# Kernel optimization log

Hardware: AMD Instinct MI355X
Metric: run time of the kernel (lower is better)

Reference implementation:

```python
import jax, jax.numpy as jnp
import numpy as np

B, C_IN, C_OUT, N = 8, 256, 256, 2048
SCALE = 10.0
EPSILON = 1e-3
LEAKY_SLOPE = 0.01
NORM_EPS = 1e-12


def setup_inputs() -> dict:
    key = jax.random.key(0)
    k1, k2, k3, k4 = jax.random.split(key, 4)
    query = jax.random.normal(k1, (B, C_IN, N), dtype=jnp.float32)
    key_t = jax.random.normal(k2, (B, C_IN, N), dtype=jnp.float32)
    # Shared key/query conv (self_attention=True), 1x1 Conv1d weights (no bias)
    fan1 = 1.0 / np.sqrt(C_IN)
    fan2 = 1.0 / np.sqrt(2 * C_IN)
    W1 = jax.random.uniform(k3, (2 * C_IN, C_IN), jnp.float32, -fan1, fan1)
    W2 = jax.random.uniform(k4, (C_OUT, 2 * C_IN), jnp.float32, -fan2, fan2)
    return {"query": query, "key": key_t, "W1": W1, "W2": W2}


def _nonlinearity(x, W1, W2):
    # 1x1 Conv1d == channel-mixing matmul; x: [B, C, N]
    h = jnp.einsum("oc,bcn->bon", W1, x)
    h = jnp.where(h >= 0, h, LEAKY_SLOPE * h)
    return jnp.einsum("oc,bcn->bon", W2, h)


def _l2norm(x):
    # F.normalize(x, dim=1): divide by max(||x||_2, eps)
    n = jnp.sqrt(jnp.sum(x * x, axis=1, keepdims=True))
    return x / jnp.maximum(n, NORM_EPS)


def reference(query, key, W1, W2):
    q_out = _l2norm(_nonlinearity(query, W1, W2))  # [B, C_out, Nq]
    k_out = _l2norm(_nonlinearity(key, W1, W2))    # [B, C_out, Nk]
    scores = jnp.einsum("bcq,bck->bqk", q_out, k_out) * SCALE  # [B, Nq, Nk]
    weights = jax.nn.softmax(scores, axis=-1)
    weights = jnp.where(weights > EPSILON, weights, 0.0)  # nn.Threshold(eps, 0)
    return (weights, key)
```

## Files before the change

### kernel.cpp

```cpp
#include <hip/hip_runtime.h>
#include <hip/hip_bf16.h>
#include <math.h>

#define B_      8
#define CIN     256
#define CMID    512
#define COUT    256
#define N_      2048
#define SCALE_  10.0f
#define EPS_THR 1e-3f
#define NORM_EPS_ 1e-12f

typedef __attribute__((ext_vector_type(8))) short short8;
typedef __attribute__((ext_vector_type(4))) float f32x4;

__device__ __forceinline__ ushort f2bf(float x) {
    union { float f; uint u; } v; v.f = x;
    uint r = v.u + 0x7FFF + ((v.u >> 16) & 1);
    return (ushort)(r >> 16);
}
__device__ __forceinline__ float bf2f(ushort h) {
    union { uint u; float f; } v; v.u = ((uint)h) << 16;
    return v.f;
}
__device__ __forceinline__ void gload_lds16(const void* g, void* l) {
    __builtin_amdgcn_global_load_lds((const __attribute__((address_space(1))) void*)g,
                                     (__attribute__((address_space(3))) void*)l, 16, 0, 0);
}

__global__ __launch_bounds__(256) void prep_w(const float* __restrict__ W1,
                                              const float* __restrict__ W2,
                                              ushort* __restrict__ W1b,
                                              ushort* __restrict__ W2b) {
    int idx = blockIdx.x * 256 + threadIdx.x;
    W1b[idx] = f2bf(W1[idx]);
    W2b[idx] = f2bf(W2[idx]);
}

#define ASTRIDE 40
__global__ __launch_bounds__(512) void conv1_fused(const float* __restrict__ q,
                                                   const float* __restrict__ k,
                                                   const ushort* __restrict__ W1b,
                                                   ushort* __restrict__ H) {
    __shared__ ushort As[64 * ASTRIDE];
    __shared__ ushort Bs[512 * 32];
    int tid = threadIdx.x;
    int lane = tid & 63, wave = tid >> 6;
    int g = lane >> 4, cl = lane & 15;
    int bx = blockIdx.x;
    int half = bx >> 8;
    int u = bx & 255;
    int pb = u & 7, pj = u >> 3;
    size_t m0 = ((size_t)half * 256 + (size_t)pb * 32 + pj) * 64;
    const float* xsrc = (m0 < 16384) ? q : k;
    int b = (int)((m0 >> 11) & 7);
    int nbase = (int)(m0 & 2047);
    const float* xp = xsrc + ((size_t)b * CIN + wave * 4) * N_ + nbase + lane;

    f32x4 acc[4][4];
#pragma unroll
    for (int i = 0; i < 4; ++i)
#pragma unroll
        for (int j = 0; j < 4; ++j) acc[i][j] = (f32x4)0.f;

    for (int k0 = 0; k0 < CIN; k0 += 32) {
#pragma unroll
        for (int si = 0; si < 4; ++si) {
            int s = tid + si * 512;
            gload_lds16(W1b + (size_t)(s >> 2) * CIN + k0 + (s & 3) * 8, Bs + s * 8);
        }
        float v0 = xp[(size_t)(k0 + 0) * N_];
        float v1 = xp[(size_t)(k0 + 1) * N_];
        float v2 = xp[(size_t)(k0 + 2) * N_];
        float v3 = xp[(size_t)(k0 + 3) * N_];
        ushort4 wv;
        wv.x = f2bf(v0); wv.y = f2bf(v1); wv.z = f2bf(v2); wv.w = f2bf(v3);
        *(ushort4*)&As[lane * ASTRIDE + wave * 4] = wv;
        __syncthreads();

        short8 af[4], bfr[4];
#pragma unroll
        for (int mi = 0; mi < 4; ++mi)
            af[mi] = *(const short8*)&As[(mi * 16 + cl) * ASTRIDE + g * 8];
#pragma unroll
        for (int ni = 0; ni < 4; ++ni)
            bfr[ni] = *(const short8*)&Bs[(wave * 64 + ni * 16 + cl) * 32 + g * 8];
#pragma unroll
        for (int mi = 0; mi < 4; ++mi)
#pragma unroll
            for (int ni = 0; ni < 4; ++ni)
                acc[mi][ni] = __builtin_amdgcn_mfma_f32_16x16x32_bf16(af[mi], bfr[ni], acc[mi][ni], 0, 0, 0);
        __syncthreads();
    }

#pragma unroll
    for (int mi = 0; mi < 4; ++mi)
#pragma unroll
        for (int ni = 0; ni < 4; ++ni)
#pragma unroll
            for (int r = 0; r < 4; ++r) {
                float v = acc[mi][ni][r];
                v = (v >= 0.f) ? v : 0.01f * v;
                H[(m0 + mi * 16 + g * 4 + r) * CMID + wave * 64 + ni * 16 + cl] = f2bf(v);
            }
}

__global__ __launch_bounds__(512) void conv2_norm(const ushort* __restrict__ H,
                                                  const ushort* __restrict__ W2b,
                                                  ushort* __restrict__ QK) {
    __shared__ ushort As[128 * 32];
    __shared__ ushort Bs[256 * 32];
    __shared__ float red[4][128];
    int tid = threadIdx.x;
    int lane = tid & 63, wave = tid >> 6;
    int wm = wave >> 2, wn = wave & 3;
    int g = lane >> 4, cl = lane & 15;
    int bx = blockIdx.x;
    int half = bx >> 7;
    int u = bx & 127;
    int pb = u & 7, pj = u >> 3;
    size_t m0 = ((size_t)half * 128 + (size_t)pb * 16 + pj) * 128;

    f32x4 acc[4][4];
#pragma unroll
    for (int i = 0; i < 4; ++i)
#pragma unroll
        for (int j = 0; j < 4; ++j) acc[i][j] = (f32x4)0.f;

    for (int k0 = 0; k0 < CMID; k0 += 32) {
        gload_lds16(H + (m0 + (tid >> 2)) * CMID + k0 + (tid & 3) * 8, As + tid * 8);
#pragma unroll
        for (int si = 0; si < 2; ++si) {
            int s = tid + si * 512;
            gload_lds16(W2b + (size_t)(s >> 2) * CMID + k0 + (s & 3) * 8, Bs + s * 8);
        }
        __syncthreads();
        short8 af[4], bfr[4];
#pragma unroll
        for (int mi = 0; mi < 4; ++mi)
            af[mi] = *(const short8*)&As[(wm * 64 + mi * 16 + cl) * 32 + g * 8];
#pragma unroll
        for (int ni = 0; ni < 4; ++ni)
            bfr[ni] = *(const short8*)&Bs[(wn * 64 + ni * 16 + cl) * 32 + g * 8];
#pragma unroll
        for (int mi = 0; mi < 4; ++mi)
#pragma unroll
            for (int ni = 0; ni < 4; ++ni)
                acc[mi][ni] = __builtin_amdgcn_mfma_f32_16x16x32_bf16(af[mi], bfr[ni], acc[mi][ni], 0, 0, 0);
        __syncthreads();
    }

#pragma unroll
    for (int mi = 0; mi < 4; ++mi)
#pragma unroll
        for (int r = 0; r < 4; ++r) {
            float s = 0.f;
#pragma unroll
            for (int ni = 0; ni < 4; ++ni) { float v = acc[mi][ni][r]; s += v * v; }
#pragma unroll
            for (int off = 1; off < 16; off <<= 1) s += __shfl_xor(s, off, 64);
            if (cl == 0) red[wn][wm * 64 + mi * 16 + g * 4 + r] = s;
        }
    __syncthreads();
#pragma unroll
    for (int mi = 0; mi < 4; ++mi)
#pragma unroll
        for (int r = 0; r < 4; ++r) {
            int row = wm * 64 + mi * 16 + g * 4 + r;
            size_t row_g = m0 + row;
            float tot = red[0][row] + red[1][row] + red[2][row] + red[3][row];
            float inv = 1.0f / fmaxf(sqrtf(tot), NORM_EPS_);
            size_t pbase = (row_g >> 4) * 4096 + (size_t)(row_g & 15) * 8;
#pragma unroll
            for (int ni = 0; ni < 4; ++ni) {
                int kcol = wn * 64 + ni * 16 + cl;
                size_t off = pbase + (size_t)(kcol >> 5) * 512
                           + (size_t)((kcol >> 3) & 3) * 128 + (kcol & 7);
                QK[off] = f2bf(acc[mi][ni][r] * inv);
            }
        }
}

#define ESTRIDE 2052
__global__ __launch_bounds__(512, 4) void scores_softmax(const ushort* __restrict__ QK,
                                                         float* __restrict__ out) {
    __shared__ ushort eLDS[16 * ESTRIDE];
    __shared__ float red[8][16];
    int bid = blockIdx.x;
    int b = bid & 7;
    int m0 = (bid >> 3) * 16;
    int tid = threadIdx.x;
    int lane = tid & 63, wave = tid >> 6;
    int g = lane >> 4, cl = lane & 15;

    const ushort* Qf = QK + ((size_t)(b * N_ + m0) >> 4) * 4096;
    const ushort* Kf = QK + ((size_t)(16384 + b * N_ + wave * 256) >> 4) * 4096;

    short8 af[8];
#pragma unroll
    for (int ks = 0; ks < 8; ++ks)
        af[ks] = *(const short8*)(Qf + ks * 512 + lane * 8);

    float rs[4] = {0.f, 0.f, 0.f, 0.f};
    int ecol = wave * 256 + cl;

#pragma unroll
    for (int ct = 0; ct < 16; ++ct) {
        f32x4 a0 = (f32x4)0.f;
#pragma unroll
        for (int ks = 0; ks < 8; ++ks) {
            short8 bfr = *(const short8*)(Kf + (size_t)ct * 4096 + ks * 512 + lane * 8);
            a0 = __builtin_amdgcn_mfma_f32_16x16x32_bf16(af[ks], bfr, a0, 0, 0, 0);
        }
#pragma unroll
        for (int r = 0; r < 4; ++r) {
            float e0 = __expf((a0[r] - 1.0f) * SCALE_);
            rs[r] += e0;
            eLDS[(g * 4 + r) * ESTRIDE + ecol + ct * 16] = f2bf(e0);
        }
    }

#pragma unroll
    for (int r = 0; r < 4; ++r) {
        float s = rs[r];
#pragma unroll
        for (int off = 1; off < 16; off <<= 1) s += __shfl_xor(s, off, 64);
        if (cl == 0) red[wave][g * 4 + r] = s;
    }
    __syncthreads();

    float inv_[2];
#pragma unroll
    for (int rr = 0; rr < 2; ++rr) {
        int row = wave * 2 + rr;
        float t = 0.f;
#pragma unroll
        for (int w = 0; w < 8; ++w) t += red[w][row];
        inv_[rr] = 1.0f / t;
    }

    float* ob = out + (size_t)b * N_ * N_ + (size_t)m0 * N_;
#pragma unroll
    for (int rr = 0; rr < 2; ++rr) {
        int row = wave * 2 + rr;
        const ushort* ep = &eLDS[row * ESTRIDE];
        float* orow = ob + (size_t)row * N_;
#pragma unroll
        for (int j = 0; j < 8; ++j) {
            int c = j * 256 + lane * 4;
            ushort4 ev = *(const ushort4*)&ep[c];
            f32x4 w;
            float t;
            t = bf2f(ev.x) * inv_[rr]; w.x = (t > EPS_THR) ? t : 0.f;
            t = bf2f(ev.y) * inv_[rr]; w.y = (t > EPS_THR) ? t : 0.f;
            t = bf2f(ev.z) * inv_[rr]; w.z = (t > EPS_THR) ? t : 0.f;
            t = bf2f(ev.w) * inv_[rr]; w.w = (t > EPS_THR) ? t : 0.f;
            __builtin_nontemporal_store(w, (f32x4*)&orow[c]);
        }
    }
}

__global__ __launch_bounds__(256) void copy_key(const float* __restrict__ in,
                                                float* __restrict__ dst, int n4) {
    int i = blockIdx.x * 256 + threadIdx.x;
    if (i < n4) {
        f32x4 v = ((const f32x4*)in)[i];
        __builtin_nontemporal_store(v, &((f32x4*)dst)[i]);
    }
}

extern "C" void kernel_launch(void* const* d_in, const int* in_sizes, int n_in,
                              void* d_out, int out_size, void* d_ws, size_t ws_size,
                              hipStream_t stream) {
    const float* q  = (const float*)d_in[0];
    const float* k  = (const float*)d_in[1];
    const float* W1 = (const float*)d_in[2];
    const float* W2 = (const float*)d_in[3];
    float* out = (float*)d_out;

    ushort* W1b = (ushort*)d_ws;
    ushort* W2b = W1b + 131072;
    ushort* QK  = W2b + 131072;

    ushort* H = (ushort*)d_out;

    prep_w<<<512, 256, 0, stream>>>(W1, W2, W1b, W2b);
    conv1_fused<<<512, 512, 0, stream>>>(q, k, W1b, H);
    conv2_norm<<<256, 512, 0, stream>>>(H, W2b, QK);
    scores_softmax<<<1024, 512, 0, stream>>>(QK, out);
    copy_key<<<4096, 256, 0, stream>>>(k, out + (size_t)B_ * N_ * N_, (B_ * CIN * N_) / 4);
}
```

Baseline: 115.3 us.

## Process four row groups per block with double-buffered LDS and overlapped stores

The scores_softmax kernel now handles 64 query rows per block in four 16-row groups instead of 16 rows, cutting the grid from 1024 to 256 blocks. Each group's exp values go to one of two LDS buffers. The normalized, thresholded stores of the previous group are interleaved with the MFMA loop of the current group, so output writes overlap compute. K fragments are loaded into registers ahead of the MFMA chain. LDS use doubles and occupancy is lowered to 2 blocks per CU, which with 256 blocks may underfill the GPU and adds register pressure.

New measurement: 211.0 us. 83.0% more time.

```diff
diff --git a/kernel.cpp b/kernel.cpp
--- a/kernel.cpp
+++ b/kernel.cpp
@@ -182,81 +182,101 @@
 }
 
 #define ESTRIDE 2052
-__global__ __launch_bounds__(512, 4) void scores_softmax(const ushort* __restrict__ QK,
+__global__ __launch_bounds__(512, 2) void scores_softmax(const ushort* __restrict__ QK,
                                                          float* __restrict__ out) {
-    __shared__ ushort eLDS[16 * ESTRIDE];
+    __shared__ ushort eLDS[2][16 * ESTRIDE];
     __shared__ float red[8][16];
     int bid = blockIdx.x;
     int b = bid & 7;
-    int m0 = (bid >> 3) * 16;
+    int m0 = (bid >> 3) * 64;
     int tid = threadIdx.x;
     int lane = tid & 63, wave = tid >> 6;
-    int g = lane >> 4, cl = lane & 15;
-
-    const ushort* Qf = QK + ((size_t)(b * N_ + m0) >> 4) * 4096;
+    int g16 = lane >> 4, cl = lane & 15;
+
     const ushort* Kf = QK + ((size_t)(16384 + b * N_ + wave * 256) >> 4) * 4096;
-
-    short8 af[8];
-#pragma unroll
-    for (int ks = 0; ks < 8; ++ks)
-        af[ks] = *(const short8*)(Qf + ks * 512 + lane * 8);
-
-    float rs[4] = {0.f, 0.f, 0.f, 0.f};
+    float* obase = out + (size_t)b * N_ * N_;
+    int srow = wave * 2 + (lane >> 5);
+    int scol0 = (lane & 31) * 4;
     int ecol = wave * 256 + cl;
 
+    float inv_[2] = {0.f, 0.f};
+    int prev_m = 0;
+
+#pragma unroll
+    for (int grp = 0; grp < 4; ++grp) {
+        int gm = m0 + grp * 16;
+        const ushort* Qf = QK + ((size_t)(b * N_ + gm) >> 4) * 4096;
+        short8 af[8];
+#pragma unroll
+        for (int ks = 0; ks < 8; ++ks)
+            af[ks] = *(const short8*)(Qf + ks * 512 + lane * 8);
+        float rs[4] = {0.f, 0.f, 0.f, 0.f};
+        ushort* ebuf = eLDS[grp & 1];
+        const ushort* pbuf = eLDS[(grp & 1) ^ 1];
+
+#pragma unroll
+        for (int ct = 0; ct < 16; ++ct) {
+            short8 bfr[8];
+#pragma unroll
+            for (int ks = 0; ks < 8; ++ks)
+                bfr[ks] = *(const short8*)(Kf + (size_t)ct * 4096 + ks * 512 + lane * 8);
+            if (grp > 0) {
+                int scol = ct * 128 + scol0;
+                ushort4 ev = *(const ushort4*)&pbuf[srow * ESTRIDE + scol];
+                float iv = inv_[lane >> 5];
+                f32x4 w;
+                float t;
+                t = bf2f(ev.x) * iv; w.x = (t > EPS_THR) ? t : 0.f;
+                t = bf2f(ev.y) * iv; w.y = (t > EPS_THR) ? t : 0.f;
+                t = bf2f(ev.z) * iv; w.z = (t > EPS_THR) ? t : 0.f;
+                t = bf2f(ev.w) * iv; w.w = (t > EPS_THR) ? t : 0.f;
+                __builtin_nontemporal_store(w, (f32x4*)&obase[(size_t)(prev_m + srow) * N_ + scol]);
+            }
+            f32x4 a0 = (f32x4)0.f;
+#pragma unroll
+            for (int ks = 0; ks < 8; ++ks)
+                a0 = __builtin_amdgcn_mfma_f32_16x16x32_bf16(af[ks], bfr[ks], a0, 0, 0, 0);
+#pragma unroll
+            for (int r = 0; r < 4; ++r) {
+                float e0 = __expf((a0[r] - 1.0f) * SCALE_);
+                rs[r] += e0;
+                ebuf[(g16 * 4 + r) * ESTRIDE + ecol + ct * 16] = f2bf(e0);
+            }
+        }
+
+#pragma unroll
+        for (int r = 0; r < 4; ++r) {
+            float s = rs[r];
+#pragma unroll
+            for (int off = 1; off < 16; off <<= 1) s += __shfl_xor(s, off, 64);
+            if (cl == 0) red[wave][g16 * 4 + r] = s;
+        }
+        __syncthreads();
+#pragma unroll
+        for (int rr = 0; rr < 2; ++rr) {
+            int row = wave * 2 + rr;
+            float t = 0.f;
+#pragma unroll
+            for (int w = 0; w < 8; ++w) t += red[w][row];
+            inv_[rr] = 1.0f / t;
+        }
+        prev_m = gm;
+        __syncthreads();
+    }
+
+    const ushort* pbuf = eLDS[1];
+    float iv = inv_[lane >> 5];
 #pragma unroll
     for (int ct = 0; ct < 16; ++ct) {
-        f32x4 a0 = (f32x4)0.f;
-#pragma unroll
-        for (int ks = 0; ks < 8; ++ks) {
-            short8 bfr = *(const short8*)(Kf + (size_t)ct * 4096 + ks * 512 + lane * 8);
-            a0 = __builtin_amdgcn_mfma_f32_16x16x32_bf16(af[ks], bfr, a0, 0, 0, 0);
-        }
-#pragma unroll
-        for (int r = 0; r < 4; ++r) {
-            float e0 = __expf((a0[r] - 1.0f) * SCALE_);
-            rs[r] += e0;
-            eLDS[(g * 4 + r) * ESTRIDE + ecol + ct * 16] = f2bf(e0);
-        }
-    }
-
-#pragma unroll
-    for (int r = 0; r < 4; ++r) {
-        float s = rs[r];
-#pragma unroll
-        for (int off = 1; off < 16; off <<= 1) s += __shfl_xor(s, off, 64);
-        if (cl == 0) red[wave][g * 4 + r] = s;
-    }
-    __syncthreads();
-
-    float inv_[2];
-#pragma unroll
-    for (int rr = 0; rr < 2; ++rr) {
-        int row = wave * 2 + rr;
-        float t = 0.f;
-#pragma unroll
-        for (int w = 0; w < 8; ++w) t += red[w][row];
-        inv_[rr] = 1.0f / t;
-    }
-
-    float* ob = out + (size_t)b * N_ * N_ + (size_t)m0 * N_;
-#pragma unroll
-    for (int rr = 0; rr < 2; ++rr) {
-        int row = wave * 2 + rr;
-        const ushort* ep = &eLDS[row * ESTRIDE];
-        float* orow = ob + (size_t)row * N_;
-#pragma unroll
-        for (int j = 0; j < 8; ++j) {
-            int c = j * 256 + lane * 4;
-            ushort4 ev = *(const ushort4*)&ep[c];
-            f32x4 w;
-            float t;
-            t = bf2f(ev.x) * inv_[rr]; w.x = (t > EPS_THR) ? t : 0.f;
-            t = bf2f(ev.y) * inv_[rr]; w.y = (t > EPS_THR) ? t : 0.f;
-            t = bf2f(ev.z) * inv_[rr]; w.z = (t > EPS_THR) ? t : 0.f;
-            t = bf2f(ev.w) * inv_[rr]; w.w = (t > EPS_THR) ? t : 0.f;
-            __builtin_nontemporal_store(w, (f32x4*)&orow[c]);
-        }
+        int scol = ct * 128 + scol0;
+        ushort4 ev = *(const ushort4*)&pbuf[srow * ESTRIDE + scol];
+        f32x4 w;
+        float t;
+        t = bf2f(ev.x) * iv; w.x = (t > EPS_THR) ? t : 0.f;
+        t = bf2f(ev.y) * iv; w.y = (t > EPS_THR) ? t : 0.f;
+        t = bf2f(ev.z) * iv; w.z = (t > EPS_THR) ? t : 0.f;
+        t = bf2f(ev.w) * iv; w.w = (t > EPS_THR) ? t : 0.f;
+        __builtin_nontemporal_store(w, (f32x4*)&obase[(size_t)(prev_m + srow) * N_ + scol]);
     }
 }
 
@@ -287,6 +307,6 @@
     prep_w<<<512, 256, 0, stream>>>(W1, W2, W1b, W2b);
     conv1_fused<<<512, 512, 0, stream>>>(q, k, W1b, H);
     conv2_norm<<<256, 512, 0, stream>>>(H, W2b, QK);
-    scores_softmax<<<1024, 512, 0, stream>>>(QK, out);
+    scores_softmax<<<256, 512, 0, stream>>>(QK, out);
     copy_key<<<4096, 256, 0, stream>>>(k, out + (size_t)B_ * N_ * N_, (B_ * CIN * N_) / 4);
 }
```
